# Optimization experiments

Hardware: AMD Instinct MI355X
Metric: run time of the kernel (lower is better)

Reference implementation:

```python
import jax, jax.numpy as jnp
import numpy as np
from jax import lax

WSIZE = 11
SIGMA = 1.5
PAD = WSIZE // 2  # 5
C1 = 0.01 ** 2
C2 = 0.03 ** 2


def _gauss1d():
    x = np.arange(WSIZE) - WSIZE // 2
    g = np.exp(-(x.astype(np.float64) ** 2) / (2.0 * SIGMA ** 2))
    g = g / g.sum()
    return jnp.asarray(g, dtype=jnp.float32)


def _blur3d(x, g):
    """Replicate-pad by 5 on D/H/W then apply the separable 11x11x11 Gaussian.
    x: [N, 1, D, H, W]. Mathematically identical to the dense conv3d in the
    original (the 3D window is an exact outer product of the 1D Gaussian)."""
    xp = jnp.pad(x, ((0, 0), (0, 0), (PAD, PAD), (PAD, PAD), (PAD, PAD)), mode='edge')
    dn = ('NCDHW', 'OIDHW', 'NCDHW')
    for kshape in ((1, 1, WSIZE, 1, 1), (1, 1, 1, WSIZE, 1), (1, 1, 1, 1, WSIZE)):
        xp = lax.conv_general_dilated(xp, g.reshape(kshape), (1, 1, 1), 'VALID',
                                      dimension_numbers=dn)
    return xp


def _rerange(img):
    img = jnp.where(img.max() > 128.0, img / 255.0, img)
    img = jnp.where(img.min() < -0.5, (img + 1.0) / 2.0, img)
    return img


def setup_inputs() -> dict:
    key = jax.random.key(0)
    k1, k2 = jax.random.split(key)
    N, C, H, W = 4, 16, 512, 512
    pred = jax.random.uniform(k1, (N, C, H, W), dtype=jnp.float32)
    gt = jax.random.uniform(k2, (N, C, H, W), dtype=jnp.float32)
    return {"pred": pred, "gt": gt}


def reference(pred, gt):
    N = pred.shape[0]
    pred = _rerange(pred)
    gt = _rerange(gt)

    # ---- PSNR (range = 1.0, reduce='sum') ----
    mse = jnp.mean((pred - gt) ** 2, axis=(1, 2, 3))           # [N]
    psnr = jnp.sum(10.0 * jnp.log10(1.0 / mse))                # scalar

    # ---- 3D SSIM over [N,1,C,H,W] volumes ----
    g = _gauss1d()
    img = pred[:, None]                                        # [N,1,D,H,W]
    gtt = gt[:, None]
    mu1 = _blur3d(img, g)
    mu2 = _blur3d(gtt, g)
    mu1_sq = mu1 * mu1
    mu2_sq = mu2 * mu2
    mu1_mu2 = mu1 * mu2
    sigma1_sq = _blur3d(img * img, g) - mu1_sq
    sigma2_sq = _blur3d(gtt * gtt, g) - mu2_sq
    sigma12 = _blur3d(img * gtt, g) - mu1_mu2

    v1 = 2.0 * sigma12 + C2
    v2 = sigma1_sq + sigma2_sq + C2
    ssim_map = ((2.0 * mu1_mu2 + C1) * v1) / ((mu1_sq + mu2_sq + C1) * v2)
    ssim = jnp.sum(jnp.mean(ssim_map, axis=(1, 2, 3, 4)))      # reduce='sum'

    return psnr, ssim, N
```

## Files before the change

### kernel.cpp

```cpp
#include <hip/hip_runtime.h>
#include <cmath>


#define NB 4
#define DD 16
#define HH 512
#define WW 512
#define SLICE (HH * WW)
#define VOL (DD * SLICE)
#define C1F 0.0001f
#define C2F 0.0009f

#define TH 16
#define TW 16
#define NTHR 256

typedef _Float16 h8 __attribute__((ext_vector_type(8)));
typedef float f4 __attribute__((ext_vector_type(4)));

__device__ inline f4 mfma16(uint4 a, uint4 b, f4 c) {
  return __builtin_amdgcn_mfma_f32_16x16x32_f16(
      __builtin_bit_cast(h8, a), __builtin_bit_cast(h8, b), c, 0, 0, 0);
}
__device__ inline unsigned pkh(float a, float b) {
  return __builtin_bit_cast(unsigned, __builtin_amdgcn_cvt_pkrtz(a, b));
}
__device__ inline int iclamp(int v, int lo, int hi) {
  return v < lo ? lo : (v > hi ? hi : v);
}

__device__ inline float block_sum256(float v) {
#pragma unroll
  for (int o = 32; o > 0; o >>= 1) v += __shfl_down(v, o, 64);
  __shared__ float r[4];
  if ((threadIdx.x & 63) == 0) r[threadIdx.x >> 6] = v;
  __syncthreads();
  float out = 0.f;
  if (threadIdx.x == 0) {
#pragma unroll
    for (int i = 0; i < 4; ++i) out += r[i];
  }
  __syncthreads();
  return out;
}

__global__ void zero_acc_k(float* acc) {
  if (threadIdx.x < 8) acc[threadIdx.x] = 0.f;
}

__global__ __launch_bounds__(NTHR, 3) void fused_k(
    const float* __restrict__ pred, const float* __restrict__ gt,
    float* __restrict__ acc, const uint4* __restrict__ tabs) {
  __shared__ _Float16 sd[4 * 32 * 40];
  __shared__ _Float16 ost[4 * 256 * 16];
  __shared__ uint4 zzq;

  int b = blockIdx.x;
  int tile = b & 1023;
  int n = b >> 10;
  int th0 = (tile >> 5) * TH;
  int tw0 = (tile & 31) * TW;
  int t = threadIdx.x;
  int lane = t & 63, wv = t >> 6;
  int lo = lane & 15, hi = lane >> 4;

  uint4 bh = tabs[lane];
  uint4 gwt = tabs[64 + lane];
  uint4 wlf = tabs[128 + lane];

  unsigned* sdw = (unsigned*)sd;
#pragma unroll
  for (int i = 0; i < 10; ++i) sdw[t + i * 256] = 0;
  if (t == 0) zzq = make_uint4(0, 0, 0, 0);

  int rp0 = t / 26, x0 = t - rp0 * 26;
  int gx0 = iclamp(tw0 + x0 - 5, 0, WW - 1);
  int go0a = iclamp(th0 + 2 * rp0 - 5, 0, HH - 1) * WW + gx0;
  int go0b = iclamp(th0 + 2 * rp0 - 4, 0, HH - 1) * WW + gx0;
  int w0 = x0 * 20 + rp0;
  bool ox0 = (x0 >= 5) && (x0 < 21);
  float o0a = (ox0 && rp0 >= 3 && rp0 <= 10) ? 1.f : 0.f;
  float o0b = (ox0 && rp0 >= 2 && rp0 <= 9) ? 1.f : 0.f;
  int i1 = t + 82;
  bool has2 = (i1 >= 256);
  int rp1 = i1 / 26, x1 = i1 - rp1 * 26;
  int gx1 = iclamp(tw0 + x1 - 5, 0, WW - 1);
  int go1a = iclamp(th0 + 2 * rp1 - 5, 0, HH - 1) * WW + gx1;
  int go1b = iclamp(th0 + 2 * rp1 - 4, 0, HH - 1) * WW + gx1;
  int w1 = x1 * 20 + rp1;
  bool ox1 = (x1 >= 5) && (x1 < 21);
  float o1a = (ox1 && rp1 >= 3 && rp1 <= 10) ? 1.f : 0.f;
  float o1b = (ox1 && rp1 >= 2 && rp1 <= 9) ? 1.f : 0.f;

  const float* pb = pred + (size_t)n * VOL;
  const float* qb = gt + (size_t)n * VOL;

  float p0a = pb[go0a], p0b = pb[go0b], q0a = qb[go0a], q0b = qb[go0b];
  float p1a = 0.f, p1b = 0.f, q1a = 0.f, q1b = 0.f;
  if (has2) { p1a = pb[go1a]; p1b = pb[go1b]; q1a = qb[go1a]; q1b = qb[go1b]; }

  int owb = wv * 1024 + (64 * hi + lo) * 4;
  int qx = 2 * (hi & 1);
  const uint4* sdq = (const uint4*)sd;
  int fr0 = wv * 160 + lo * 5 + hi;
  int fr1 = wv * 160 + (lo + 16) * 5 + hi;
  f4 z4 = {0.f, 0.f, 0.f, 0.f};

  float psnr = 0.f;
  float oe0, oe1, oe2, oe3;
  unsigned pA0, pA1, pA2, pA3, pB0, pB1, pB2, pB3;
  oe0 = oe1 = oe2 = oe3 = 0.f;
  pA0 = pA1 = pA2 = pA3 = pB0 = pB1 = pB2 = pB3 = 0u;

  __syncthreads();

#pragma unroll 1
  for (int d = 0; d < DD; ++d) {
    {
      float SA = p0a + q0a, DA = p0a - q0a;
      float SB = p0b + q0b, DB = p0b - q0b;
      float dA = DA * DA, dB = DB * DB;
      psnr = fmaf(o0a, dA, psnr);
      psnr = fmaf(o0b, dB, psnr);
      sdw[w0]        = pkh(SA, SB);
      sdw[640 + w0]  = pkh(DA, DB);
      sdw[1280 + w0] = pkh(SA * SA, SB * SB);
      sdw[1920 + w0] = pkh(dA, dB);
    }
    if (has2) {
      float SA = p1a + q1a, DA = p1a - q1a;
      float SB = p1b + q1b, DB = p1b - q1b;
      float dA = DA * DA, dB = DB * DB;
      psnr = fmaf(o1a, dA, psnr);
      psnr = fmaf(o1b, dB, psnr);
      sdw[w1]        = pkh(SA, SB);
      sdw[640 + w1]  = pkh(DA, DB);
      sdw[1280 + w1] = pkh(SA * SA, SB * SB);
      sdw[1920 + w1] = pkh(dA, dB);
    }
    __syncthreads();

    uint4 fa0 = sdq[fr0];
    uint4 fa1 = sdq[fr1];
    __syncthreads();

    if (d < DD - 1) {
      const float* P = pb + (size_t)(d + 1) * SLICE;
      const float* Q = qb + (size_t)(d + 1) * SLICE;
      p0a = P[go0a]; p0b = P[go0b]; q0a = Q[go0a]; q0b = Q[go0b];
      if (has2) { p1a = P[go1a]; p1b = P[go1b]; q1a = Q[go1a]; q1b = Q[go1b]; }
    }

    f4 t0 = mfma16(fa0, bh, z4);
    f4 t1 = mfma16(fa1, bh, z4);
    uint4 ta = make_uint4(pkh(t0.x, t0.y), pkh(t0.z, t0.w),
                          pkh(t1.x, t1.y), pkh(t1.z, t1.w));
    f4 o = mfma16(ta, gwt, z4);

    if ((d & 1) == 0) {
      oe0 = o.x; oe1 = o.y; oe2 = o.z; oe3 = o.w;
    } else if ((d & 2) == 0) {
      pA0 = pkh(oe0, o.x); pA1 = pkh(oe1, o.y);
      pA2 = pkh(oe2, o.z); pA3 = pkh(oe3, o.w);
    } else {
      pB0 = pkh(oe0, o.x); pB1 = pkh(oe1, o.y);
      pB2 = pkh(oe2, o.z); pB3 = pkh(oe3, o.w);
      int Qp = (d >> 2) ^ qx;
      uint2* op = (uint2*)ost;
      op[owb + Qp]       = make_uint2(pA0, pB0);
      op[owb + 64 + Qp]  = make_uint2(pA1, pB1);
      op[owb + 128 + Qp] = make_uint2(pA2, pB2);
      op[owb + 192 + Qp] = make_uint2(pA3, pB3);
    }
  }
  __syncthreads();

  const uint4* oq = (const uint4*)ost;
  int bnt = wv & 1;
  int blk = (hi < 2) ? (hi ^ bnt) : 0;
  bool real = (hi < 2);
  float ssum = 0.f;
#pragma unroll
  for (int q = 0; q < 4; ++q) {
    int nt = 4 * wv + q;
    int bidx = (16 * nt + lo) * 2 + blk;
    const uint4* bp0 = real ? &oq[bidx] : &zzq;
    const uint4* bp1 = real ? &oq[512 + bidx] : &zzq;
    const uint4* bp2 = real ? &oq[1024 + bidx] : &zzq;
    const uint4* bp3 = real ? &oq[1536 + bidx] : &zzq;
    f4 cS = mfma16(wlf, *bp0, z4);
    f4 cD = mfma16(wlf, *bp1, z4);
    f4 cS2 = mfma16(wlf, *bp2, z4);
    f4 cD2 = mfma16(wlf, *bp3, z4);
#pragma unroll
    for (int r = 0; r < 4; ++r) {
      float Sb = cS[r], Db = cD[r], B1 = cS2[r], B2 = cD2[r];
      float SS = Sb * Sb, DDm = Db * Db;
      float m12_2 = (SS - DDm) * 0.5f;
      float msq = (SS + DDm) * 0.5f;
      float Epq = (B1 - B2) * 0.25f;
      float Esum = (B1 + B2) * 0.5f;
      float sig12_2 = 2.f * Epq - m12_2;
      float svar = Esum - msq;
      float num = (m12_2 + C1F) * (sig12_2 + C2F);
      float den = (msq + C1F) * (svar + C2F);
      ssum += num / den;
    }
  }
  float bs = block_sum256(ssum);
  if (t == 0) atomicAdd(&acc[4 + n], bs);
  float bp = block_sum256(psnr);
  if (t == 0) atomicAdd(&acc[n], bp);
}

__global__ void final_k(const float* __restrict__ acc, float* __restrict__ out) {
  if (threadIdx.x == 0 && blockIdx.x == 0) {
    double psnr = 0.0, ssim = 0.0;
    for (int n = 0; n < NB; ++n) {
      double mse = (double)acc[n] / (double)VOL;
      psnr += 10.0 * log10(1.0 / mse);
      ssim += (double)acc[4 + n] / (double)VOL;
    }
    out[0] = (float)psnr;
    out[1] = (float)ssim;
    out[2] = (float)NB;
  }
}

static unsigned short f2h(float f) {
  union { float f; unsigned u; } v; v.f = f;
  unsigned u = v.u;
  unsigned s = (u >> 16) & 0x8000u;
  int e = (int)((u >> 23) & 0xff) - 127 + 15;
  unsigned m = u & 0x7fffffu;
  if (e <= 0) return (unsigned short)s;
  if (e >= 31) return (unsigned short)(s | 0x7c00u);
  unsigned h = ((unsigned)e << 10) | (m >> 13);
  unsigned rem = m & 0x1fffu;
  if (rem > 0x1000u || (rem == 0x1000u && (h & 1u))) h++;
  return (unsigned short)(s | h);
}
static float h2f(unsigned short h) {
  unsigned se = (h >> 10) & 0x1f, m = h & 0x3ffu, s = ((unsigned)h & 0x8000u) << 16;
  union { unsigned u; float f; } v;
  if (se == 0) { v.u = s; return v.f; }
  v.u = s | ((se - 15 + 127) << 23) | (m << 13);
  return v.f;
}

static unsigned s_tabs[192 * 4];
static bool s_init = false;

extern "C" void kernel_launch(void* const* d_in, const int* in_sizes, int n_in,
                              void* d_out, int out_size, void* d_ws, size_t ws_size,
                              hipStream_t stream) {
  const float* pred = (const float*)d_in[0];
  const float* gt = (const float*)d_in[1];
  float* acc = (float*)d_ws;

  if (!s_init) {
    double tt[11], s = 0.0;
    for (int i = 0; i < 11; ++i) {
      double x = i - 5;
      tt[i] = exp(-(x * x) / 4.5);
      s += tt[i];
    }
    float g[11];
    for (int i = 0; i < 11; ++i) g[i] = (float)(tt[i] / s);
    unsigned short hg[11];
    for (int i = 0; i < 11; ++i) hg[i] = f2h(g[i]);
    for (int pass = 0; pass < 3; ++pass) {
      double sum = 0.0;
      for (int i = 0; i < 11; ++i) sum += (double)h2f(hg[i]);
      hg[5] = f2h((float)((double)h2f(hg[5]) + (1.0 - sum)));
    }
    float wl[DD][DD];
    for (int o = 0; o < DD; ++o)
      for (int d = 0; d < DD; ++d) {
        float w = 0.f;
        for (int k = 0; k < 11; ++k) {
          int j = o + k - 5;
          j = j < 0 ? 0 : (j > 15 ? 15 : j);
          if (j == d) w += g[k];
        }
        wl[d][o] = w;
      }
    unsigned short wlh[DD][DD];
    for (int o = 0; o < DD; ++o) {
      int dmx = 0;
      for (int d = 0; d < DD; ++d) {
        wlh[o][d] = f2h(wl[d][o]);
        if (wl[d][o] > wl[dmx][o]) dmx = d;
      }
      for (int pass = 0; pass < 3; ++pass) {
        double sum = 0.0;
        for (int d = 0; d < DD; ++d) sum += (double)h2f(wlh[o][d]);
        wlh[o][dmx] = f2h((float)((double)h2f(wlh[o][dmx]) + (1.0 - sum)));
      }
    }
    for (int l = 0; l < 64; ++l) {
      int lo = l & 15, hi = l >> 4;
      unsigned short v[8];
      for (int i = 0; i < 8; ++i) {
        int idx = 8 * hi + i - lo;
        v[i] = (idx >= 0 && idx <= 10) ? hg[idx] : 0;
      }
      for (int k = 0; k < 4; ++k)
        s_tabs[l * 4 + k] = (unsigned)v[2 * k] | ((unsigned)v[2 * k + 1] << 16);
      for (int i = 0; i < 8; ++i) {
        int c = 4 * hi + (i & 3) + 16 * (i >> 2);
        int idx = c - lo;
        v[i] = (idx >= 0 && idx <= 10) ? hg[idx] : 0;
      }
      for (int k = 0; k < 4; ++k)
        s_tabs[(64 + l) * 4 + k] = (unsigned)v[2 * k] | ((unsigned)v[2 * k + 1] << 16);
      for (int i = 0; i < 8; ++i)
        v[i] = (hi < 2) ? wlh[lo][8 * hi + i] : 0;
      for (int k = 0; k < 4; ++k)
        s_tabs[(128 + l) * 4 + k] = (unsigned)v[2 * k] | ((unsigned)v[2 * k + 1] << 16);
    }
    s_init = true;
  }

  hipMemcpyAsync((char*)d_ws + 64, s_tabs, sizeof(s_tabs),
                 hipMemcpyHostToDevice, stream);
  zero_acc_k<<<1, 64, 0, stream>>>(acc);
  fused_k<<<NB * 1024, NTHR, 0, stream>>>(pred, gt, acc,
                                          (const uint4*)((char*)d_ws + 64));
  final_k<<<1, 1, 0, stream>>>(acc, (float*)d_out);
}
```

Baseline: 295.2 us.

## Double-buffer LDS staging and transpose 2D blur layout to drop a barrier

The per-slice staging buffer becomes two ping-pong buffers, so the second __syncthreads after the fragment reads is removed. The loader mapping changes to pack column pairs instead of row pairs, and the MFMA operand order of the second pass is swapped to match. The tables in tabs are renamed and must now hold matching coefficients. LDS use grows, which may affect occupancy at the 3-blocks-per-CU launch bound.

```diff
diff --git a/kernel.cpp b/kernel.cpp
--- a/kernel.cpp
+++ b/kernel.cpp
@@ -10,9 +10,6 @@
 #define VOL (DD * SLICE)
 #define C1F 0.0001f
 #define C2F 0.0009f
-
-#define TH 16
-#define TW 16
 #define NTHR 256
 
 typedef _Float16 h8 __attribute__((ext_vector_type(8)));
@@ -51,59 +48,58 @@
 __global__ __launch_bounds__(NTHR, 3) void fused_k(
     const float* __restrict__ pred, const float* __restrict__ gt,
     float* __restrict__ acc, const uint4* __restrict__ tabs) {
-  __shared__ _Float16 sd[4 * 32 * 40];
+  __shared__ _Float16 sd[2 * 4 * 32 * 32];
   __shared__ _Float16 ost[4 * 256 * 16];
   __shared__ uint4 zzq;
 
   int b = blockIdx.x;
   int tile = b & 1023;
   int n = b >> 10;
-  int th0 = (tile >> 5) * TH;
-  int tw0 = (tile & 31) * TW;
+  int th0 = (tile >> 5) * 16;
+  int tw0 = (tile & 31) * 16;
   int t = threadIdx.x;
   int lane = t & 63, wv = t >> 6;
   int lo = lane & 15, hi = lane >> 4;
 
-  uint4 bh = tabs[lane];
-  uint4 gwt = tabs[64 + lane];
+  uint4 gstd = tabs[lane];
+  uint4 gpck = tabs[64 + lane];
   uint4 wlf = tabs[128 + lane];
 
   unsigned* sdw = (unsigned*)sd;
 #pragma unroll
-  for (int i = 0; i < 10; ++i) sdw[t + i * 256] = 0;
+  for (int i = 0; i < 16; ++i) sdw[t + i * 256] = 0;
   if (t == 0) zzq = make_uint4(0, 0, 0, 0);
 
-  int rp0 = t / 26, x0 = t - rp0 * 26;
-  int gx0 = iclamp(tw0 + x0 - 5, 0, WW - 1);
-  int go0a = iclamp(th0 + 2 * rp0 - 5, 0, HH - 1) * WW + gx0;
-  int go0b = iclamp(th0 + 2 * rp0 - 4, 0, HH - 1) * WW + gx0;
-  int w0 = x0 * 20 + rp0;
-  bool ox0 = (x0 >= 5) && (x0 < 21);
-  float o0a = (ox0 && rp0 >= 3 && rp0 <= 10) ? 1.f : 0.f;
-  float o0b = (ox0 && rp0 >= 2 && rp0 <= 9) ? 1.f : 0.f;
+  int r0 = t / 13, cp0 = t - r0 * 13;
+  int gy0 = iclamp(th0 + r0 - 5, 0, HH - 1);
+  int ga0 = gy0 * WW + iclamp(tw0 + 2 * cp0 - 5, 0, WW - 1);
+  int gb0 = gy0 * WW + iclamp(tw0 + 2 * cp0 - 4, 0, WW - 1);
+  int w0 = r0 * 16 + cp0;
+  bool orow0 = (r0 >= 5) && (r0 <= 20);
+  float o0a = (orow0 && cp0 >= 3 && cp0 <= 10) ? 1.f : 0.f;
+  float o0b = (orow0 && cp0 >= 2 && cp0 <= 9) ? 1.f : 0.f;
   int i1 = t + 82;
-  bool has2 = (i1 >= 256);
-  int rp1 = i1 / 26, x1 = i1 - rp1 * 26;
-  int gx1 = iclamp(tw0 + x1 - 5, 0, WW - 1);
-  int go1a = iclamp(th0 + 2 * rp1 - 5, 0, HH - 1) * WW + gx1;
-  int go1b = iclamp(th0 + 2 * rp1 - 4, 0, HH - 1) * WW + gx1;
-  int w1 = x1 * 20 + rp1;
-  bool ox1 = (x1 >= 5) && (x1 < 21);
-  float o1a = (ox1 && rp1 >= 3 && rp1 <= 10) ? 1.f : 0.f;
-  float o1b = (ox1 && rp1 >= 2 && rp1 <= 9) ? 1.f : 0.f;
+  bool has2 = (i1 >= NTHR);
+  int r1 = i1 / 13, cp1 = i1 - r1 * 13;
+  int gy1 = iclamp(th0 + r1 - 5, 0, HH - 1);
+  int ga1 = gy1 * WW + iclamp(tw0 + 2 * cp1 - 5, 0, WW - 1);
+  int gb1 = gy1 * WW + iclamp(tw0 + 2 * cp1 - 4, 0, WW - 1);
+  int w1 = r1 * 16 + cp1;
+  bool orow1 = (r1 >= 5) && (r1 <= 20);
+  float o1a = (orow1 && cp1 >= 3 && cp1 <= 10) ? 1.f : 0.f;
+  float o1b = (orow1 && cp1 >= 2 && cp1 <= 9) ? 1.f : 0.f;
 
   const float* pb = pred + (size_t)n * VOL;
   const float* qb = gt + (size_t)n * VOL;
 
-  float p0a = pb[go0a], p0b = pb[go0b], q0a = qb[go0a], q0b = qb[go0b];
+  float p0a = pb[ga0], p0b = pb[gb0], q0a = qb[ga0], q0b = qb[gb0];
   float p1a = 0.f, p1b = 0.f, q1a = 0.f, q1b = 0.f;
-  if (has2) { p1a = pb[go1a]; p1b = pb[go1b]; q1a = qb[go1a]; q1b = qb[go1b]; }
+  if (has2) { p1a = pb[ga1]; p1b = pb[gb1]; q1a = qb[ga1]; q1b = qb[gb1]; }
 
   int owb = wv * 1024 + (64 * hi + lo) * 4;
   int qx = 2 * (hi & 1);
+  int fb = wv * 128 + lo * 4 + hi;
   const uint4* sdq = (const uint4*)sd;
-  int fr0 = wv * 160 + lo * 5 + hi;
-  int fr1 = wv * 160 + (lo + 16) * 5 + hi;
   f4 z4 = {0.f, 0.f, 0.f, 0.f};
 
   float psnr = 0.f;
@@ -116,16 +112,17 @@
 
 #pragma unroll 1
   for (int d = 0; d < DD; ++d) {
+    unsigned* sb = sdw + (d & 1) * 2048;
     {
       float SA = p0a + q0a, DA = p0a - q0a;
       float SB = p0b + q0b, DB = p0b - q0b;
       float dA = DA * DA, dB = DB * DB;
       psnr = fmaf(o0a, dA, psnr);
       psnr = fmaf(o0b, dB, psnr);
-      sdw[w0]        = pkh(SA, SB);
-      sdw[640 + w0]  = pkh(DA, DB);
-      sdw[1280 + w0] = pkh(SA * SA, SB * SB);
-      sdw[1920 + w0] = pkh(dA, dB);
+      sb[w0]        = pkh(SA, SB);
+      sb[512 + w0]  = pkh(DA, DB);
+      sb[1024 + w0] = pkh(SA * SA, SB * SB);
+      sb[1536 + w0] = pkh(dA, dB);
     }
     if (has2) {
       float SA = p1a + q1a, DA = p1a - q1a;
@@ -133,29 +130,28 @@
       float dA = DA * DA, dB = DB * DB;
       psnr = fmaf(o1a, dA, psnr);
       psnr = fmaf(o1b, dB, psnr);
-      sdw[w1]        = pkh(SA, SB);
-      sdw[640 + w1]  = pkh(DA, DB);
-      sdw[1280 + w1] = pkh(SA * SA, SB * SB);
-      sdw[1920 + w1] = pkh(dA, dB);
-    }
-    __syncthreads();
-
-    uint4 fa0 = sdq[fr0];
-    uint4 fa1 = sdq[fr1];
+      sb[w1]        = pkh(SA, SB);
+      sb[512 + w1]  = pkh(DA, DB);
+      sb[1024 + w1] = pkh(SA * SA, SB * SB);
+      sb[1536 + w1] = pkh(dA, dB);
+    }
     __syncthreads();
 
     if (d < DD - 1) {
       const float* P = pb + (size_t)(d + 1) * SLICE;
       const float* Q = qb + (size_t)(d + 1) * SLICE;
-      p0a = P[go0a]; p0b = P[go0b]; q0a = Q[go0a]; q0b = Q[go0b];
-      if (has2) { p1a = P[go1a]; p1b = P[go1b]; q1a = Q[go1a]; q1b = Q[go1b]; }
-    }
-
-    f4 t0 = mfma16(fa0, bh, z4);
-    f4 t1 = mfma16(fa1, bh, z4);
+      p0a = P[ga0]; p0b = P[gb0]; q0a = Q[ga0]; q0b = Q[gb0];
+      if (has2) { p1a = P[ga1]; p1b = P[gb1]; q1a = Q[ga1]; q1b = Q[gb1]; }
+    }
+
+    uint4 fa0 = sdq[(d & 1) * 512 + fb];
+    uint4 fa1 = sdq[(d & 1) * 512 + fb + 64];
+
+    f4 t0 = mfma16(fa0, gstd, z4);
+    f4 t1 = mfma16(fa1, gstd, z4);
     uint4 ta = make_uint4(pkh(t0.x, t0.y), pkh(t0.z, t0.w),
                           pkh(t1.x, t1.y), pkh(t1.z, t1.w));
-    f4 o = mfma16(ta, gwt, z4);
+    f4 o = mfma16(gpck, ta, z4);
 
     if ((d & 1) == 0) {
       oe0 = o.x; oe1 = o.y; oe2 = o.z; oe3 = o.w;
```

Result: no change. 299.5 us (+1.5%).
